# Optimization experiments

Hardware: AMD Instinct MI355X
Metric: run time of the kernel (lower is better)

The kernel has to match this reference:

```python
import jax, jax.numpy as jnp
import numpy as np

EPS = 1e-5        # BatchNorm eps (torch default)
SLOPE = 0.2       # LeakyReLU negative slope
K_DIL, K_DIL_POS, K = 8, 6, 32


def _sqdist(a):
    # a: (B,N,D) -> squared pairwise distances (B,N,N); monotone in cdist(p=2)
    n = jnp.sum(a * a, axis=-1)
    return n[:, :, None] + n[:, None, :] - 2.0 * jnp.einsum('bnd,bmd->bnm', a, a)


def _knn(a, k):
    # k nearest neighbors excluding self (drop the closest = self, as in torch topk[..., 1:])
    _, idx = jax.lax.top_k(-_sqdist(a), k + 1)
    return idx[:, :, 1:]  # (B,N,k) int32


def _edge_feat(x, idx):
    # x: (B,N,C), idx: (B,N,K) -> (B,N,K,2C) = concat(neighbor - center, center)
    B = x.shape[0]
    b_idx = jnp.arange(B)[:, None, None]
    nbr = x[b_idx, idx]                       # (B,N,K,C) gather
    ctr = x[:, :, None, :]                    # (B,N,1,C)
    ctr_b = jnp.broadcast_to(ctr, nbr.shape)
    return jnp.concatenate([nbr - ctr, ctr_b], axis=-1)


def _conv_bn_lrelu(f, W, g, b):
    # 1x1 Conv2d (no bias) + BatchNorm2d(track_running_stats=False, batch stats) + LeakyReLU(0.2)
    # f: (B,N,K,Cin), W: (Cout,Cin)
    y = jnp.einsum('bnkc,oc->bnko', f, W)
    mu = jnp.mean(y, axis=(0, 1, 2))
    var = jnp.var(y, axis=(0, 1, 2))          # biased var, as torch BN normalization
    y = (y - mu) * jax.lax.rsqrt(var + EPS) * g + b
    return jnp.where(y > 0, y, SLOPE * y)


def setup_inputs() -> dict:
    key = jax.random.key(0)
    ks = jax.random.split(key, 8)
    B, N, C, D = 2, 4096, 64, 3
    hidden, out_c = 128, 64
    c1 = 2 * C   # convdilated channels
    c2 = 4 * C   # conv input channels (edge feature of 2C-dim features)
    return {
        'x': jax.random.normal(ks[0], (B, N, C), jnp.float32),
        'pos': jax.random.normal(ks[1], (B, N, D), jnp.float32),
        'W1': jax.random.normal(ks[2], (c1, c1), jnp.float32) * 0.05,
        'g1': jnp.ones((c1,), jnp.float32),
        'b1': jnp.zeros((c1,), jnp.float32),
        'W2': jax.random.normal(ks[3], (hidden, c2), jnp.float32) * 0.05,
        'g2': jnp.ones((hidden,), jnp.float32),
        'b2': jnp.zeros((hidden,), jnp.float32),
        'W3': jax.random.normal(ks[4], (out_c, hidden), jnp.float32) * 0.05,
        'g3': jnp.ones((out_c,), jnp.float32),
        'b3': jnp.zeros((out_c,), jnp.float32),
    }


def reference(x, pos, W1, g1, b1, W2, g2, b2, W3, g3, b3):
    # Dual graph 1: feature-KNN (k_dilated) concat pos-KNN (k_dilated_pos)
    idx1 = jnp.concatenate([_knn(x, K_DIL), _knn(pos, K_DIL_POS)], axis=2)  # (B,N,14)
    f1 = _edge_feat(x, idx1)                                                # (B,N,14,2C)
    h1 = jnp.max(_conv_bn_lrelu(f1, W1, g1, b1), axis=2)                    # (B,N,2C)
    # Graph 2: k_pos == 0 -> pure position KNN
    idx2 = _knn(pos, K)                                                     # (B,N,32)
    f2 = _edge_feat(h1, idx2)                                               # (B,N,32,4C)
    h2 = _conv_bn_lrelu(f2, W2, g2, b2)                                     # (B,N,32,hidden)
    h3 = _conv_bn_lrelu(h2, W3, g3, b3)                                     # (B,N,32,out)
    out = jnp.max(h3, axis=2)                                               # (B,N,out)
    return out, idx2
```

## Files before the change

kernel.cpp:

```cpp
#include <hip/hip_runtime.h>
#include <hip/hip_bf16.h>
#include <type_traits>

using bf16 = __hip_bfloat16;

namespace {

constexpr int B_ = 2;
constexpr int N_ = 4096;
constexpr int C_ = 64;
constexpr int K14_ = 14;
constexpr int KX_ = 8;
constexpr int KP_ = 6;
constexpr int K2_ = 32;
constexpr int OC_ = 64;

__device__ __forceinline__ float bflo(unsigned u) { return __uint_as_float(u << 16); }
__device__ __forceinline__ float bfhi(unsigned u) { return __uint_as_float(u & 0xffff0000u); }

__device__ __forceinline__ unsigned pack_f16(float a, float b) {
  _Float16 ha = (_Float16)a, hb = (_Float16)b;
  unsigned short ua = __builtin_bit_cast(unsigned short, ha);
  unsigned short ub = __builtin_bit_cast(unsigned short, hb);
  return (unsigned)ua | ((unsigned)ub << 16);
}

using half2v = __attribute__((ext_vector_type(2))) _Float16;
__device__ __forceinline__ float dot2(unsigned a, unsigned b, float acc) {
  float out;
  asm("v_dot2_f32_f16 %0, %1, %2, %3" : "=v"(out) : "v"(a), "v"(b), "v"(acc));
  return out;
}

__device__ __forceinline__ unsigned fmono(float d) {
  unsigned u = __float_as_uint(d);
  return u ^ (((int)u < 0) ? 0xFFFFFFFFu : 0x80000000u);
}

#define GRP8_ONE(GV, GS, T) \
  { bool av = !((taken >> (T)) & 1ull); float dv_ = DSTV(T); bool bb = av && dv_ < GV; \
    GV = bb ? dv_ : GV; GS = bb ? (T) : GS; }
#define GRP8(GV, GS, B) do { GV = 3.0e38f; GS = B; \
  GRP8_ONE(GV, GS, (B)+0) GRP8_ONE(GV, GS, (B)+1) GRP8_ONE(GV, GS, (B)+2) \
  GRP8_ONE(GV, GS, (B)+3) GRP8_ONE(GV, GS, (B)+4) GRP8_ONE(GV, GS, (B)+5) \
  GRP8_ONE(GV, GS, (B)+6) GRP8_ONE(GV, GS, (B)+7) } while (0)
#define GTREE_ONE(GV, GS) { bool bb = GV < pv; pv = bb ? GV : pv; ptt = bb ? GS : ptt; }
#define GTREE() do { pv = gv0; ptt = gs0; \
  GTREE_ONE(gv1, gs1) GTREE_ONE(gv2, gs2) GTREE_ONE(gv3, gs3) GTREE_ONE(gv4, gs4) \
  GTREE_ONE(gv5, gs5) GTREE_ONE(gv6, gs6) GTREE_ONE(gv7, gs7) } while (0)
#define GRP_SWITCH(TT) do { switch ((TT) >> 3) { \
  case 0: GRP8(gv0, gs0, 0);  break; case 1: GRP8(gv1, gs1, 8);  break; \
  case 2: GRP8(gv2, gs2, 16); break; case 3: GRP8(gv3, gs3, 24); break; \
  case 4: GRP8(gv4, gs4, 32); break; case 5: GRP8(gv5, gs5, 40); break; \
  case 6: GRP8(gv6, gs6, 48); break; case 7: GRP8(gv7, gs7, 56); break; } \
  GTREE(); } while (0)
#define SEL_DECL float gv0, gv1, gv2, gv3, gv4, gv5, gv6, gv7; \
  int gs0, gs1, gs2, gs3, gs4, gs5, gs6, gs7; float pv; int ptt; \
  unsigned long long taken = 0ull;
#define SEL_INIT do { \
  GRP8(gv0, gs0, 0);  GRP8(gv1, gs1, 8);  GRP8(gv2, gs2, 16); GRP8(gv3, gs3, 24); \
  GRP8(gv4, gs4, 32); GRP8(gv5, gs5, 40); GRP8(gv6, gs6, 48); GRP8(gv7, gs7, 56); \
  GTREE(); } while (0)

__global__ __launch_bounds__(256)
void xnorm_kernel(const float* __restrict__ x, float* __restrict__ nx)
{
  int p = blockIdx.x * 256 + threadIdx.x;
  if (p >= B_ * N_) return;
  float s = 0.f;
#pragma unroll 8
  for (int c = 0; c < C_; ++c) { float v = x[p * C_ + c]; s = fmaf(v, v, s); }
  nx[p] = s;
}

__global__ __launch_bounds__(256)
void wprep_kernel(const float* __restrict__ W1, const float* __restrict__ W2,
                  const float* __restrict__ W3,
                  float* __restrict__ WT1a, float* __restrict__ WT1bm,
                  float* __restrict__ WT2a, float* __restrict__ WT2bm,
                  unsigned* __restrict__ w3p)
{
  int idx = blockIdx.x * 256 + threadIdx.x;
  if (idx < 128 * 128) {
    int o = idx & 127, c = idx >> 7;
    float a = W2[o * 256 + c];
    WT2a[c * 128 + o] = a;
    WT2bm[c * 128 + o] = W2[o * 256 + 128 + c] - a;
    if (c < 64) {
      float a1 = W1[o * 128 + c];
      WT1a[c * 128 + o] = a1;
      WT1bm[c * 128 + o] = W1[o * 128 + 64 + c] - a1;
    }
  }
  if (idx < 64 * 64) {
    int oo = idx & 63, c2 = idx >> 6;
    w3p[c2 * 64 + oo] = pack_f16(W3[oo * 128 + 2 * c2], W3[oo * 128 + 2 * c2 + 1]);
  }
}

__global__ __launch_bounds__(256)
void knn_x_kernel(const float* __restrict__ x, const float* __restrict__ nx,
                  int* __restrict__ idx1)
{
  __shared__ unsigned tileh[256 * 33];
  const int wave = threadIdx.x >> 6, lane = threadIdx.x & 63;
  const int qg = blockIdx.x * 4 + wave;
  const int bb = qg >> 12;
  const float* xb = x + bb * N_ * C_;
  unsigned myq;
  {
    float2 qv = *(const float2*)&x[qg * C_ + 2 * (lane & 31)];
    myq = pack_f16(qv.x, qv.y);
  }
  unsigned qp[32];
#pragma unroll
  for (int c2 = 0; c2 < 32; ++c2) qp[c2] = __builtin_amdgcn_readlane(myq, c2);
  const float nq = nx[qg];
  const float* nb_ = nx + bb * N_;
  float dst[64];
#pragma unroll
  for (int ti = 0; ti < 16; ++ti) {
    __syncthreads();
    for (int e = threadIdx.x; e < 256 * 32; e += 256) {
      int c2 = e & 31, j = e >> 5;
      float2 v = *(const float2*)&xb[(ti * 256 + j) * C_ + 2 * c2];
      tileh[j * 33 + c2] = pack_f16(v.x, v.y);
    }
    __syncthreads();
#pragma unroll
    for (int nb4 = 0; nb4 < 4; ++nb4) {
      const unsigned* row = &tileh[(nb4 * 64 + lane) * 33];
      float acc = 0.f;
#pragma unroll
      for (int c2 = 0; c2 < 32; ++c2) acc = dot2(qp[c2], row[c2], acc);
      float nbv = nb_[ti * 256 + nb4 * 64 + lane];
      dst[ti * 4 + nb4] = nq + nbv - 2.f * acc;
    }
  }
#define DSTV(T) dst[T]
  SEL_DECL;
  SEL_INIT;
  for (int r = 0; r < KX_ + 1; ++r) {
    int j = ((ptt >> 2) << 8) + ((ptt & 3) << 6) + lane;
    unsigned long long key = ((unsigned long long)fmono(pv) << 32) | (unsigned)j;
#pragma unroll
    for (int m = 1; m < 64; m <<= 1) {
      unsigned long long ok = __shfl_xor(key, m, 64);
      key = ok < key ? ok : key;
    }
    int wj = (int)(key & 0xFFFFFFFFull);
    if (r > 0 && lane == 0) idx1[qg * K14_ + (r - 1)] = wj;
    if ((wj & 63) == lane) {
      int tt = ((wj >> 8) << 2) | ((wj >> 6) & 3);
      taken |= 1ull << tt;
      GRP_SWITCH(tt);
    }
  }
#undef DSTV
}

__global__ __launch_bounds__(256)
void knn_pos_kernel(const float* __restrict__ pos,
                    int* __restrict__ idx1, int* __restrict__ idx2,
                    float* __restrict__ oidx)
{
#pragma clang fp contract(off)
  __shared__ float pL[3][N_];
  __shared__ float nL[N_];
  const int wave = threadIdx.x >> 6, lane = threadIdx.x & 63;
  const int qg = blockIdx.x * 4 + wave;
  const int bb = qg >> 12;
  const float* pb = pos + bb * N_ * 3;
  for (int j = threadIdx.x; j < N_; j += 256) {
    float a = pb[j * 3], b = pb[j * 3 + 1], c = pb[j * 3 + 2];
    pL[0][j] = a; pL[1][j] = b; pL[2][j] = c;
    float aa = a * a;
    float bb2 = b * b;
    float cc = c * c;
    float s1 = aa + bb2;
    nL[j] = s1 + cc;
  }
  __syncthreads();
  const int q = qg & (N_ - 1);
  const float qx = pL[0][q], qy = pL[1][q], qz = pL[2][q];
  const float nq = nL[q];
  float dst[64];
#pragma unroll
  for (int t = 0; t < 64; ++t) {
    int j = t * 64 + lane;
    float dot = qx * pL[0][j];
    dot = fmaf(qy, pL[1][j], dot);
    dot = fmaf(qz, pL[2][j], dot);
    float t1 = nq + nL[j];
    float t2 = 2.0f * dot;
    dst[t] = t1 - t2;
  }
#define DSTV(T) dst[T]
  SEL_DECL;
  SEL_INIT;
  for (int r = 0; r < K2_ + 1; ++r) {
    int j = ptt * 64 + lane;
    unsigned long long key = ((unsigned long long)fmono(pv) << 32) | (unsigned)j;
#pragma unroll
    for (int m = 1; m < 64; m <<= 1) {
      unsigned long long ok = __shfl_xor(key, m, 64);
      key = ok < key ? ok : key;
    }
    int wj = (int)(key & 0xFFFFFFFFull);
    if (r > 0 && lane == 0) {
      int rr = r - 1;
      if (rr < KP_) idx1[qg * K14_ + KX_ + rr] = wj;
      idx2[qg * K2_ + rr] = wj;
      oidx[qg * K2_ + rr] = (float)wj;
    }
    if ((wj & 63) == lane) {
      int tt = wj >> 6;
      taken |= 1ull << tt;
      GRP_SWITCH(tt);
    }
  }
#undef DSTV
}

template<int CIN, typename TIN>
__global__ __launch_bounds__(256)
void lin_kernel(const TIN* __restrict__ in, const float* __restrict__ WT,
                bf16* __restrict__ out)
{
  __shared__ float wt[CIN * 128];
  for (int e = threadIdx.x; e < CIN * 128; e += 256) wt[e] = WT[e];
  __syncthreads();
  const int which = threadIdx.x >> 7, o = threadIdx.x & 127;
  for (int p0 = blockIdx.x * 2; p0 < B_ * N_; p0 += gridDim.x * 2) {
    int p = p0 + which;
    float acc = 0.f;
#pragma unroll 8
    for (int c = 0; c < CIN; ++c) {
      float v;
      if constexpr (std::is_same_v<TIN, float>) v = in[p * CIN + c];
      else v = __bfloat162float(in[p * CIN + c]);
      acc = fmaf(wt[c * 128 + o], v, acc);
    }
    out[p * 128 + o] = __float2bfloat16(acc);
  }
}

template<int KNB>
__global__ __launch_bounds__(256)
void stats_gather_kernel(const bf16* __restrict__ a, const bf16* __restrict__ ac,
                         const int* __restrict__ nbr, double* __restrict__ st)
{
  const int o = threadIdx.x & 127;
  const int which = threadIdx.x >> 7;
  double s = 0.0, s2 = 0.0;
  for (int p0 = blockIdx.x * 2; p0 < B_ * N_; p0 += gridDim.x * 2) {
    int p = p0 + which;
    int base = (p >> 12) << 12;
    float acv = __bfloat162float(ac[p * 128 + o]);
#pragma unroll 2
    for (int kk = 0; kk < KNB; ++kk) {
      int nb = nbr[p * KNB + kk] & (N_ - 1);
      float y = __bfloat162float(a[(base + nb) * 128 + o]) + acv;
      s += (double)y; s2 += (double)y * (double)y;
    }
  }
  atomicAdd(&st[o], s);
  atomicAdd(&st[128 + o], s2);
}

__global__ void bnfin_kernel(const double* __restrict__ st, const float* __restrict__ g,
                             const float* __restrict__ bi, float* __restrict__ so,
                             int nch, double cnt)
{
  int o = threadIdx.x;
  if (o >= nch) return;
  double mu = st[o] / cnt;
  double var = st[nch + o] / cnt - mu * mu;
  double sc = (double)g[o] / sqrt(var + 1e-5);
  so[o] = (float)sc;
  so[nch + o] = (float)((double)bi[o] - mu * sc);
}

__global__ __launch_bounds__(256)
void h1_kernel(const bf16* __restrict__ u, const bf16* __restrict__ uc,
               const int* __restrict__ idx1, const float* __restrict__ so,
               bf16* __restrict__ h1)
{
  const int o = threadIdx.x & 127, which = threadIdx.x >> 7;
  float sc = so[o], off = so[128 + o];
  for (int p0 = blockIdx.x * 2; p0 < B_ * N_; p0 += gridDim.x * 2) {
    int p = p0 + which;
    int base = (p >> 12) << 12;
    float ucv = __bfloat162float(uc[p * 128 + o]);
    float m = -3.0e38f;
#pragma unroll
    for (int kk = 0; kk < K14_; ++kk) {
      int nb = idx1[p * K14_ + kk] & (N_ - 1);
      float y = __bfloat162float(u[(base + nb) * 128 + o]) + ucv;
      float v = fmaf(y, sc, off);
      v = v > 0.f ? v : 0.2f * v;
      m = fmaxf(m, v);
    }
    h1[p * 128 + o] = __float2bfloat16(m);
  }
}

__global__ __launch_bounds__(256, 5)
void conv3s_kernel(const bf16* __restrict__ z, const bf16* __restrict__ zc,
                   const int* __restrict__ idx2, const float* __restrict__ so2,
                   const unsigned* __restrict__ w3p,
                   double* __restrict__ st3, unsigned* __restrict__ y3m)
{
  __shared__ unsigned w3s[64 * 64];
  __shared__ unsigned h2s[4][512];
  {
    const uint4* src = (const uint4*)w3p;
    uint4* dst4 = (uint4*)w3s;
    for (int e = threadIdx.x; e < 1024; e += 256) dst4[e] = src[e];
  }
  __syncthreads();
  const int wave = threadIdx.x >> 6, lane = threadIdx.x & 63;
  unsigned* h2w = &h2s[wave][0];
  const int swz = (lane >> 2) & 7;
  const float sclo = so2[2 * lane],       schi = so2[2 * lane + 1];
  const float offlo = so2[128 + 2 * lane], offhi = so2[129 + 2 * lane];
  double s = 0.0, s2 = 0.0;
  const int gw = blockIdx.x * 4 + wave;
  const int stride = gridDim.x * 4;
  for (int p = gw; p < B_ * N_; p += stride) {
    const int base = (p >> 12) << 12;
    const int* idxp = &idx2[p * K2_];
    const unsigned zcv = *(const unsigned*)&zc[p * 128 + 2 * lane];
    const float zclo = bflo(zcv), zchi = bfhi(zcv);
    unsigned zv[8];
#pragma unroll
    for (int i = 0; i < 8; ++i) {
      int nb = idxp[i] & (N_ - 1);
      zv[i] = *(const unsigned*)&z[(base + nb) * 128 + 2 * lane];
    }
    float mx = -3.0e38f, mn = 3.0e38f;
#pragma unroll
    for (int kc = 0; kc < 4; ++kc) {
      asm volatile("s_waitcnt lgkmcnt(0)" ::: "memory");
#pragma unroll
      for (int i = 0; i < 8; ++i) {
        float y0 = bflo(zv[i]) + zclo;
        float y1 = bfhi(zv[i]) + zchi;
        float v0 = fmaf(y0, sclo, offlo); v0 = v0 > 0.f ? v0 : 0.2f * v0;
        float v1 = fmaf(y1, schi, offhi); v1 = v1 > 0.f ? v1 : 0.2f * v1;
        h2w[(lane << 3) | (i ^ swz)] = pack_f16(v0, v1);
      }
      if (kc < 3) {
#pragma unroll
        for (int i = 0; i < 8; ++i) {
          int nb = idxp[(kc + 1) * 8 + i] & (N_ - 1);
          zv[i] = *(const unsigned*)&z[(base + nb) * 128 + 2 * lane];
        }
      }
      asm volatile("s_waitcnt lgkmcnt(0)" ::: "memory");
      float a0 = 0.f, a1 = 0.f, a2 = 0.f, a3 = 0.f;
      float a4 = 0.f, a5 = 0.f, a6 = 0.f, a7 = 0.f;
#pragma unroll
      for (int c2 = 0; c2 < 64; ++c2) {
        const int cs = (c2 >> 2) & 7;
        unsigned wp = w3s[(c2 << 6) | lane];
        uint4 ra = *(const uint4*)&h2w[c2 << 3];
        uint4 rb = *(const uint4*)&h2w[(c2 << 3) + 4];
        unsigned hv[8] = {ra.x, ra.y, ra.z, ra.w, rb.x, rb.y, rb.z, rb.w};
        a0 = dot2(wp, hv[0 ^ cs], a0);
        a1 = dot2(wp, hv[1 ^ cs], a1);
        a2 = dot2(wp, hv[2 ^ cs], a2);
        a3 = dot2(wp, hv[3 ^ cs], a3);
        a4 = dot2(wp, hv[4 ^ cs], a4);
        a5 = dot2(wp, hv[5 ^ cs], a5);
        a6 = dot2(wp, hv[6 ^ cs], a6);
        a7 = dot2(wp, hv[7 ^ cs], a7);
      }
      s += (double)a0 + (double)a1 + (double)a2 + (double)a3
         + (double)a4 + (double)a5 + (double)a6 + (double)a7;
      s2 += (double)a0 * a0 + (double)a1 * a1 + (double)a2 * a2 + (double)a3 * a3
          + (double)a4 * a4 + (double)a5 * a5 + (double)a6 * a6 + (double)a7 * a7;
      mx = fmaxf(mx, fmaxf(fmaxf(a0, a1), fmaxf(a2, a3)));
      mx = fmaxf(mx, fmaxf(fmaxf(a4, a5), fmaxf(a6, a7)));
      mn = fminf(mn, fminf(fminf(a0, a1), fminf(a2, a3)));
      mn = fminf(mn, fminf(fminf(a4, a5), fminf(a6, a7)));
    }
    y3m[p * OC_ + lane] = pack_f16(mx, mn);
  }
  atomicAdd(&st3[lane], s);
  atomicAdd(&st3[64 + lane], s2);
}

__global__ __launch_bounds__(256)
void fin3_kernel(const unsigned* __restrict__ y3m, const float* __restrict__ so3,
                 float* __restrict__ outp)
{
  int idx = blockIdx.x * 256 + threadIdx.x;
  if (idx >= B_ * N_ * OC_) return;
  int oo = idx & 63;
  float sc3 = so3[oo], off3 = so3[64 + oo];
  half2v hv = __builtin_bit_cast(half2v, y3m[idx]);
  float pick = (sc3 >= 0.f) ? (float)hv[0] : (float)hv[1];
  float v = fmaf(pick, sc3, off3);
  outp[idx] = v > 0.f ? v : 0.2f * v;
}

}

extern "C" void kernel_launch(void* const* d_in, const int* in_sizes, int n_in,
                              void* d_out, int out_size, void* d_ws, size_t ws_size,
                              hipStream_t stream) {
  const float* x   = (const float*)d_in[0];
  const float* pos = (const float*)d_in[1];
  const float* W1  = (const float*)d_in[2];
  const float* g1  = (const float*)d_in[3];
  const float* b1  = (const float*)d_in[4];
  const float* W2  = (const float*)d_in[5];
  const float* g2  = (const float*)d_in[6];
  const float* b2  = (const float*)d_in[7];
  const float* W3  = (const float*)d_in[8];
  const float* g3  = (const float*)d_in[9];
  const float* b3  = (const float*)d_in[10];

  float* outp = (float*)d_out;
  float* oidx = outp + B_ * N_ * OC_;

  char* w = (char*)d_ws;
  double* stats = (double*)w;            w += 640 * sizeof(double);
  float* nxf    = (float*)w;             w += B_ * N_ * 4;
  float* WT1a   = (float*)w;             w += 64 * 128 * 4;
  float* WT1bm  = (float*)w;             w += 64 * 128 * 4;
  float* WT2a   = (float*)w;             w += 128 * 128 * 4;
  float* WT2bm  = (float*)w;             w += 128 * 128 * 4;
  unsigned* w3p = (unsigned*)w;          w += 64 * 64 * 4;
  float* so1    = (float*)w;             w += 256 * 4;
  float* so2    = (float*)w;             w += 256 * 4;
  float* so3    = (float*)w;             w += 128 * 4;
  int* idx1     = (int*)w;               w += B_ * N_ * K14_ * 4;
  int* idx2i    = (int*)w;               w += B_ * N_ * K2_ * 4;
  bf16* u       = (bf16*)w;              w += B_ * N_ * 128 * 2;
  bf16* uc      = (bf16*)w;              w += B_ * N_ * 128 * 2;
  bf16* h1      = (bf16*)w;              w += B_ * N_ * 128 * 2;
  bf16* zz  = u;
  bf16* zzc = uc;
  unsigned* y3m = (unsigned*)h1;

  hipMemsetAsync(stats, 0, 640 * sizeof(double), stream);

  xnorm_kernel<<<(B_ * N_ + 255) / 256, 256, 0, stream>>>(x, nxf);
  wprep_kernel<<<64, 256, 0, stream>>>(W1, W2, W3, WT1a, WT1bm, WT2a, WT2bm, w3p);

  knn_x_kernel<<<2048, 256, 0, stream>>>(x, nxf, idx1);
  knn_pos_kernel<<<2048, 256, 0, stream>>>(pos, idx1, idx2i, oidx);

  lin_kernel<64, float><<<2048, 256, 0, stream>>>(x, WT1a, u);
  lin_kernel<64, float><<<2048, 256, 0, stream>>>(x, WT1bm, uc);

  stats_gather_kernel<K14_><<<2048, 256, 0, stream>>>(u, uc, idx1, stats);
  bnfin_kernel<<<1, 128, 0, stream>>>(stats, g1, b1, so1, 128, (double)(B_ * N_ * K14_));
  h1_kernel<<<2048, 256, 0, stream>>>(u, uc, idx1, so1, h1);

  lin_kernel<128, bf16><<<2048, 256, 0, stream>>>(h1, WT2a, zz);
  lin_kernel<128, bf16><<<2048, 256, 0, stream>>>(h1, WT2bm, zzc);

  stats_gather_kernel<K2_><<<2048, 256, 0, stream>>>(zz, zzc, idx2i, stats + 256);
  bnfin_kernel<<<1, 128, 0, stream>>>(stats + 256, g2, b2, so2, 128, (double)(B_ * N_ * K2_));

  conv3s_kernel<<<2048, 256, 0, stream>>>(zz, zzc, idx2i, so2, w3p, stats + 512, y3m);
  bnfin_kernel<<<1, 128, 0, stream>>>(stats + 512, g3, b3, so3, 64, (double)(B_ * N_ * K2_));
  fin3_kernel<<<B_ * N_ * OC_ / 256, 256, 0, stream>>>(y3m, so3, outp);
}
```

Measured before the change: 850.3 us.

## Fuse paired linear kernels, recompute pos norms inline, split dot accumulators

Merges the two per-point linear projections that share the same input into one kernel that computes both outputs, reading the input once and reading weights straight from global/L2 rather than staging them in shared memory. In the position KNN kernel, point norms are recomputed per element instead of being held in a shared-memory array, which saves LDS space and one load per element at the cost of a few extra flops. The feature KNN dot product uses two independent accumulators to shorten the dependency chain. Together these target launch count, redundant input reads and latency chains, but they give up the shared-memory weight cache and may change rounding slightly.

```diff
diff --git a/kernel.cpp b/kernel.cpp
--- a/kernel.cpp
+++ b/kernel.cpp
@@ -130,9 +130,13 @@
 #pragma unroll
     for (int nb4 = 0; nb4 < 4; ++nb4) {
       const unsigned* row = &tileh[(nb4 * 64 + lane) * 33];
-      float acc = 0.f;
-#pragma unroll
-      for (int c2 = 0; c2 < 32; ++c2) acc = dot2(qp[c2], row[c2], acc);
+      float accA = 0.f, accB = 0.f;
+#pragma unroll
+      for (int c2 = 0; c2 < 32; c2 += 2) {
+        accA = dot2(qp[c2], row[c2], accA);
+        accB = dot2(qp[c2 + 1], row[c2 + 1], accB);
+      }
+      float acc = accA + accB;
       float nbv = nb_[ti * 256 + nb4 * 64 + lane];
       dst[ti * 4 + nb4] = nq + nbv - 2.f * acc;
     }
@@ -166,32 +170,36 @@
 {
 #pragma clang fp contract(off)
   __shared__ float pL[3][N_];
-  __shared__ float nL[N_];
   const int wave = threadIdx.x >> 6, lane = threadIdx.x & 63;
   const int qg = blockIdx.x * 4 + wave;
   const int bb = qg >> 12;
   const float* pb = pos + bb * N_ * 3;
   for (int j = threadIdx.x; j < N_; j += 256) {
-    float a = pb[j * 3], b = pb[j * 3 + 1], c = pb[j * 3 + 2];
-    pL[0][j] = a; pL[1][j] = b; pL[2][j] = c;
-    float aa = a * a;
-    float bb2 = b * b;
-    float cc = c * c;
-    float s1 = aa + bb2;
-    nL[j] = s1 + cc;
+    pL[0][j] = pb[j * 3];
+    pL[1][j] = pb[j * 3 + 1];
+    pL[2][j] = pb[j * 3 + 2];
   }
   __syncthreads();
   const int q = qg & (N_ - 1);
   const float qx = pL[0][q], qy = pL[1][q], qz = pL[2][q];
-  const float nq = nL[q];
+  float nq;
+  {
+    float aa = qx * qx, bb2 = qy * qy, cc = qz * qz;
+    float s1 = aa + bb2;
+    nq = s1 + cc;
+  }
   float dst[64];
 #pragma unroll
   for (int t = 0; t < 64; ++t) {
     int j = t * 64 + lane;
-    float dot = qx * pL[0][j];
-    dot = fmaf(qy, pL[1][j], dot);
-    dot = fmaf(qz, pL[2][j], dot);
-    float t1 = nq + nL[j];
+    float px = pL[0][j], py = pL[1][j], pz = pL[2][j];
+    float aa = px * px, bb2 = py * py, cc = pz * pz;
+    float s1 = aa + bb2;
+    float nj = s1 + cc;
+    float dot = qx * px;
+    dot = fmaf(qy, py, dot);
+    dot = fmaf(qz, pz, dot);
+    float t1 = nq + nj;
     float t2 = 2.0f * dot;
     dst[t] = t1 - t2;
   }
@@ -224,24 +232,24 @@
 
 template<int CIN, typename TIN>
 __global__ __launch_bounds__(256)
-void lin_kernel(const TIN* __restrict__ in, const float* __restrict__ WT,
-                bf16* __restrict__ out)
-{
-  __shared__ float wt[CIN * 128];
-  for (int e = threadIdx.x; e < CIN * 128; e += 256) wt[e] = WT[e];
-  __syncthreads();
+void lin2_kernel(const TIN* __restrict__ in, const float* __restrict__ WTa,
+                 const float* __restrict__ WTb,
+                 bf16* __restrict__ outa, bf16* __restrict__ outb)
+{
   const int which = threadIdx.x >> 7, o = threadIdx.x & 127;
   for (int p0 = blockIdx.x * 2; p0 < B_ * N_; p0 += gridDim.x * 2) {
     int p = p0 + which;
-    float acc = 0.f;
-#pragma unroll 8
+    float aa = 0.f, ab = 0.f;
+#pragma unroll 4
     for (int c = 0; c < CIN; ++c) {
       float v;
       if constexpr (std::is_same_v<TIN, float>) v = in[p * CIN + c];
       else v = __bfloat162float(in[p * CIN + c]);
-      acc = fmaf(wt[c * 128 + o], v, acc);
-    }
-    out[p * 128 + o] = __float2bfloat16(acc);
+      aa = fmaf(WTa[c * 128 + o], v, aa);
+      ab = fmaf(WTb[c * 128 + o], v, ab);
+    }
+    outa[p * 128 + o] = __float2bfloat16(aa);
+    outb[p * 128 + o] = __float2bfloat16(ab);
   }
 }
 
@@ -453,15 +461,13 @@
   knn_x_kernel<<<2048, 256, 0, stream>>>(x, nxf, idx1);
   knn_pos_kernel<<<2048, 256, 0, stream>>>(pos, idx1, idx2i, oidx);
 
-  lin_kernel<64, float><<<2048, 256, 0, stream>>>(x, WT1a, u);
-  lin_kernel<64, float><<<2048, 256, 0, stream>>>(x, WT1bm, uc);
+  lin2_kernel<64, float><<<1024, 256, 0, stream>>>(x, WT1a, WT1bm, u, uc);
 
   stats_gather_kernel<K14_><<<2048, 256, 0, stream>>>(u, uc, idx1, stats);
   bnfin_kernel<<<1, 128, 0, stream>>>(stats, g1, b1, so1, 128, (double)(B_ * N_ * K14_));
   h1_kernel<<<2048, 256, 0, stream>>>(u, uc, idx1, so1, h1);
 
-  lin_kernel<128, bf16><<<2048, 256, 0, stream>>>(h1, WT2a, zz);
-  lin_kernel<128, bf16><<<2048, 256, 0, stream>>>(h1, WT2bm, zzc);
+  lin2_kernel<128, bf16><<<1024, 256, 0, stream>>>(h1, WT2a, WT2bm, zz, zzc);
 
   stats_gather_kernel<K2_><<<2048, 256, 0, stream>>>(zz, zzc, idx2i, stats + 256);
   bnfin_kernel<<<1, 128, 0, stream>>>(stats + 256, g2, b2, so2, 128, (double)(B_ * N_ * K2_));
```

Measured after the change: 838.8 us. Within noise of the previous version (-1.4%).
